# Kernel tuning notes

Hardware: AMD Instinct MI355X
Metric: run time of the kernel (lower is better)

Reference implementation:

```python
import jax, jax.numpy as jnp
import numpy as np

H = 64        # hidden_size
G = 64        # global_hidden_size
VOCAB = 128   # VOCAB_SIZE
NUM_OPS = 20
DEPTH = 12    # complete binary tree: 2**DEPTH - 1 nodes
B = 128       # batch of trees
TEMP = 3.0    # self.temperature


def setup_inputs() -> dict:
    key = jax.random.key(0)
    ks = jax.random.split(key, 16)
    s = 0.05
    N = 2 ** DEPTH - 1
    inp = {
        "x_idx": jax.random.randint(ks[0], (B, N), 0, VOCAB, dtype=jnp.int32),
        "validity_mask": jnp.ones((NUM_OPS,), jnp.float32),
        # binary tree-LSTM (blstm): x one-hot -> gates [i, f_a, f_b, o, u]
        "Wx": jax.random.normal(ks[1], (VOCAB, 5 * H), jnp.float32) * s,
        "Ua": jax.random.normal(ks[2], (H, 5 * H), jnp.float32) * s,
        "Ub": jax.random.normal(ks[3], (H, 5 * H), jnp.float32) * s,
        "b_tree": jnp.zeros((5 * H,), jnp.float32),
        # global nn.LSTM (1 layer), gate order i,f,g,o
        "W_ih": jax.random.normal(ks[4], (H, 4 * G), jnp.float32) * s,
        "W_hh": jax.random.normal(ks[5], (G, 4 * G), jnp.float32) * s,
        "b_lstm": jnp.zeros((4 * G,), jnp.float32),
        # FFN on root hidden
        "W1": jax.random.normal(ks[6], (H, H), jnp.float32) * s,
        "b1": jnp.zeros((H,), jnp.float32),
        "W2": jax.random.normal(ks[7], (H, H), jnp.float32) * s,
        "b2": jnp.zeros((H,), jnp.float32),
        # actor head on [hidden ; global_hidden]
        "actor_W": jax.random.normal(ks[8], (H + G, NUM_OPS), jnp.float32) * s,
        "actor_b": jnp.zeros((NUM_OPS,), jnp.float32),
    }
    return inp


def _tree_lstm_sweep(x_idx, Wx, Ua, Ub, b_tree):
    """Bottom-up binary tree-LSTM over a complete binary tree.
    Node i's children sit at flat positions 2i+1, 2i+2 (level layout)."""
    h_prev = c_prev = None
    for d in range(DEPTH - 1, -1, -1):
        n = 2 ** d
        off = n - 1
        # memory-bound gather of gate pre-activations: [B, n, 5H]
        z = Wx[x_idx[:, off:off + n]] + b_tree
        if h_prev is not None:
            h_a, h_b = h_prev[:, 0::2], h_prev[:, 1::2]
            c_a, c_b = c_prev[:, 0::2], c_prev[:, 1::2]
            z = z + jnp.einsum("bnh,hg->bng", h_a, Ua) + jnp.einsum("bnh,hg->bng", h_b, Ub)
        i, fa, fb, o, u = jnp.split(z, 5, axis=-1)
        c = jax.nn.sigmoid(i) * jnp.tanh(u)
        if h_prev is not None:
            c = c + jax.nn.sigmoid(fa) * c_a + jax.nn.sigmoid(fb) * c_b
        h = jax.nn.sigmoid(o) * jnp.tanh(c)
        h_prev, c_prev = h, c
    return h_prev[:, 0]  # root hidden [B, H]


def reference(x_idx, validity_mask, Wx, Ua, Ub, b_tree, W_ih, W_hh, b_lstm,
              W1, b1, W2, b2, actor_W, actor_b):
    h_root = _tree_lstm_sweep(x_idx, Wx, Ua, Ub, b_tree)
    # internal op 1: apply_ffn then apply_global_lstm
    f = jnp.maximum(h_root @ W1 + b1, 0.0) @ W2 + b2          # FFN [B, H]
    h0 = jnp.zeros((f.shape[0], G), f.dtype)
    g = f @ W_ih + h0 @ W_hh + b_lstm                          # one LSTM step
    i, fg, gg, o = jnp.split(g, 4, axis=-1)                    # torch order i,f,g,o
    c_g = jax.nn.sigmoid(i) * jnp.tanh(gg)                     # c0 = 0
    h_g = jax.nn.sigmoid(o) * jnp.tanh(c_g)                    # [B, G]
    # external actor with validity-masked weights (as in policy())
    feats = jnp.concatenate([f, h_g], axis=-1)                 # [B, H+G]
    logits = jnp.log(validity_mask) + feats @ (actor_W * validity_mask) + actor_b * validity_mask
    return jax.nn.softmax(logits / TEMP, axis=-1)              # [B, NUM_OPS]
```

## Files before the change

kernel.cpp:

```cpp
#include <hip/hip_runtime.h>


typedef unsigned short u16;
typedef unsigned int   u32;
typedef __attribute__((ext_vector_type(8))) short  short8;
typedef __attribute__((ext_vector_type(4))) float  floatx4;

#define L2E  1.44269504f
#define L2E2 2.885390082f

__device__ __forceinline__ float frcp(float x) { return __fdividef(1.0f, x); }
__device__ __forceinline__ float fsig(float x) { return frcp(1.0f + __expf(-x)); }
__device__ __forceinline__ float ftanh(float x) {
    return 1.0f - 2.0f * frcp(__expf(2.0f * x) + 1.0f);
}
__device__ __forceinline__ u16 f2bfa(float x) {
    return (u16)((__float_as_uint(x) + 0x8000u) >> 16);
}
__device__ __forceinline__ float bflo(u32 cc) { return __uint_as_float(cc << 16); }
__device__ __forceinline__ float bfhi(u32 cc) { return __uint_as_float(cc & 0xFFFF0000u); }

__device__ __forceinline__ void lstm_gates(
    float zi, float zfa, float zfb, float zo, float zu,
    float ca, float cb, float& c, float& h)
{
    zi  = fmaxf(zi, -60.f);  zfa = fmaxf(zfa, -60.f);
    zfb = fmaxf(zfb, -60.f); zo  = fmaxf(zo, -60.f);
    zu  = fmaxf(zu, -60.f);
    float ei  = __builtin_amdgcn_exp2f(-zi);
    float efa = __builtin_amdgcn_exp2f(-zfa);
    float efb = __builtin_amdgcn_exp2f(-zfb);
    float eo  = __builtin_amdgcn_exp2f(-zo);
    float eu2 = __builtin_amdgcn_exp2f(-zu);
    float pfa = 1.f + efa, pfb = 1.f + efb;
    float cf = (ca * pfb + cb * pfa) * __builtin_amdgcn_rcpf(pfa * pfb);
    c = (1.f - eu2) * __builtin_amdgcn_rcpf((1.f + ei) * (1.f + eu2)) + cf;
    float ec2 = __builtin_amdgcn_exp2f(fminf(-c * L2E2, 80.f));
    h = (1.f - ec2) * __builtin_amdgcn_rcpf((1.f + eo) * (1.f + ec2));
}

#define HS 72

__global__ void precompute_kernel(
    const float* __restrict__ Wx, const float* __restrict__ b_tree,
    const float* __restrict__ Ua, const float* __restrict__ Ub,
    float4* __restrict__ WpA, float* __restrict__ WpU,
    float4* __restrict__ TaA, float2* __restrict__ TaUC,
    float4* __restrict__ TbA, float2* __restrict__ TbUC,
    u16* __restrict__ Uswz)
{
    int v = blockIdx.x;
    int t = threadIdx.x;
    __shared__ float sz[320], sta[320], stb[320], sh[64], sc[64];
    float z = Wx[v * 320 + t] + b_tree[t];
    sz[t] = z;
    {
        int f = v * 320 + t;
        int j = f & 7, lane = (f >> 3) & 63, tk = f >> 9;
        int nt = tk % 20, kc = tk / 20;
        int k = kc * 32 + (lane >> 4) * 8 + j;
        int nn = nt * 16 + (lane & 15);
        float uval = (k < 64) ? Ua[k * 320 + nn] : Ub[(k - 64) * 320 + nn];
        uval *= ((nn >> 6) == 4) ? L2E2 : L2E;
        Uswz[f] = (u16)((__float_as_uint(uval) + 0x7FFFu +
                         ((__float_as_uint(uval) >> 16) & 1u)) >> 16);
    }
    __syncthreads();
    if (t < 64) {
        float c = fsig(sz[t]) * ftanh(sz[256 + t]);
        float h = fsig(sz[192 + t]) * ftanh(c);
        sc[t] = c; sh[t] = h;
    }
    __syncthreads();
    float ta = 0.f, tb = 0.f;
    #pragma unroll 8
    for (int k = 0; k < 64; ++k) {
        ta += sh[k] * Ua[k * 320 + t];
        tb += sh[k] * Ub[k * 320 + t];
    }
    sta[t] = ta; stb[t] = tb;
    __syncthreads();
    if (t < 64) {
        int o = (v << 6) + t;
        WpA[o]  = make_float4(sz[t] * L2E, sz[64 + t] * L2E,
                              sz[128 + t] * L2E, sz[192 + t] * L2E);
        WpU[o]  = sz[256 + t] * L2E2;
        TaA[o]  = make_float4(sta[t] * L2E, sta[64 + t] * L2E,
                              sta[128 + t] * L2E, sta[192 + t] * L2E);
        TaUC[o] = make_float2(sta[256 + t] * L2E2, sc[t]);
        TbA[o]  = make_float4(stb[t] * L2E, stb[64 + t] * L2E,
                              stb[128 + t] * L2E, stb[192 + t] * L2E);
        TbUC[o] = make_float2(stb[256 + t] * L2E2, sc[t]);
    }
}

template<int NT, int MODE, int GSRC>
__device__ __forceinline__ void sweep_level(
    const u16* hsrc, const u32* csrc,
    u16* hdst, u16* cdst, u16* hg, u16* cg, float* hroot,
    const short8 Bfrag[4][5],
    const float4* __restrict__ WpA, const float* __restrict__ WpU,
    const int* ids, int lbase, int node0g, int nvalid,
    int lane15, int quad, int wg)
{
    floatx4 acc[NT][5];
    #pragma unroll
    for (int mt = 0; mt < NT; ++mt)
        #pragma unroll
        for (int g = 0; g < 5; ++g) acc[mt][g] = (floatx4){0.f, 0.f, 0.f, 0.f};

    #pragma unroll
    for (int mt = 0; mt < NT; ++mt) {
        #pragma unroll
        for (int kc = 0; kc < 4; ++kc) {
            int child = 2 * (lbase + mt * 16 + lane15) + (kc >> 1);
            const u16* ap = GSRC ? (hsrc + child * 64 + (kc & 1) * 32 + quad * 8)
                                 : (hsrc + child * HS + (kc & 1) * 32 + quad * 8);
            short8 a = *(const short8*)ap;
            #pragma unroll
            for (int g = 0; g < 5; ++g)
                acc[mt][g] = __builtin_amdgcn_mfma_f32_16x16x32_bf16(
                    a, Bfrag[kc][g], acc[mt][g], 0, 0, 0);
        }
    }
    int hh = wg * 16 + lane15;
    #pragma unroll
    for (int mt = 0; mt < NT; ++mt) {
        #pragma unroll
        for (int r = 0; r < 4; ++r) {
            int lrow = lbase + mt * 16 + quad * 4 + r;
            int id = ids[lrow];
            float4 wgv = WpA[(id << 6) + hh];
            float  wu  = WpU[(id << 6) + hh];
            u32 cc = csrc[lrow * 64 + hh];
            float c, h;
            lstm_gates(acc[mt][0][r] + wgv.x, acc[mt][1][r] + wgv.y,
                       acc[mt][2][r] + wgv.z, acc[mt][3][r] + wgv.w,
                       acc[mt][4][r] + wu, bflo(cc), bfhi(cc), c, h);
            if (MODE == 0) {
                hdst[lrow * HS + hh] = f2bfa(h);
                cdst[(lrow >> 1) * 128 + hh * 2 + (lrow & 1)] = f2bfa(c);
            }
            if (MODE == 1) {
                if (lrow < nvalid) {
                    int node = node0g + lrow;
                    hg[node * 64 + hh] = f2bfa(h);
                    cg[(node >> 1) * 128 + hh * 2 + (node & 1)] = f2bfa(c);
                }
            }
            if (MODE == 2) {
                if (lrow == 0) hroot[hh] = h;
            }
        }
    }
}

__device__ __forceinline__ void load_bfrags(short8 Bfrag[4][5],
                                            const u16* __restrict__ Uswz,
                                            int wg, int lane)
{
    #pragma unroll
    for (int kc = 0; kc < 4; ++kc)
        #pragma unroll
        for (int g = 0; g < 5; ++g) {
            int nt = g * 4 + wg;
            Bfrag[kc][g] = *(const short8*)(Uswz + ((kc * 20 + nt) * 64 + lane) * 8);
        }
}

__global__ __launch_bounds__(512, 2) void sweepA_kernel(
    const int* __restrict__ x_idx,
    const float4* __restrict__ WpA, const float* __restrict__ WpU,
    const float4* __restrict__ TaA, const float2* __restrict__ TaUC,
    const float4* __restrict__ TbA, const float2* __restrict__ TbUC,
    const u16* __restrict__ Uswz,
    u16* __restrict__ h3, u16* __restrict__ c3)
{
    __shared__ u16 hA[128 * HS];
    __shared__ u16 cA[64 * 128];
    __shared__ u16 hB[64 * HS];
    __shared__ u16 cB[32 * 128];
    __shared__ int sIds[544];
    int t = threadIdx.x, lane = t & 63, wv = t >> 6;
    int wg = wv & 3, wm = wv >> 2;
    int lane15 = lane & 15, quad = lane >> 4;
    int b = blockIdx.x >> 3, st = blockIdx.x & 7;
    const int* xb = x_idx + b * 4095;

    for (int i = t; i < 544; i += 512) {
        int g;
        if      (i < 128) g = 1023 + st * 128 + i;
        else if (i < 384) g = 2047 + st * 256 + (i - 128);
        else if (i < 448) g = 511 + st * 64 + (i - 384);
        else if (i < 480) g = 255 + st * 32 + (i - 448);
        else if (i < 496) g = 127 + st * 16 + (i - 480);
        else if (i < 504) g = 63 + st * 8 + (i - 496);
        else if (i < 508) g = 31 + st * 4 + (i - 504);
        else if (i < 510) g = 15 + st * 2 + (i - 508);
        else if (i == 510) g = 7 + st;
        else g = -1;
        sIds[i] = (g >= 0) ? xb[g] : 0;
    }
    __syncthreads();

    #pragma unroll 4
    for (int rr = 0; rr < 16; ++rr) {
        int rl = wv * 16 + rr;
        int id = sIds[rl], ida = sIds[128 + 2 * rl], idb = sIds[129 + 2 * rl];
        float4 wgv = WpA[(id << 6) + lane];  float  wu = WpU[(id << 6) + lane];
        float4 ga = TaA[(ida << 6) + lane];  float2 ua = TaUC[(ida << 6) + lane];
        float4 gb = TbA[(idb << 6) + lane];  float2 ub = TbUC[(idb << 6) + lane];
        float c, h;
        lstm_gates(wgv.x + ga.x + gb.x, wgv.y + ga.y + gb.y, wgv.z + ga.z + gb.z,
                   wgv.w + ga.w + gb.w, wu + ua.x + ub.x, ua.y, ub.y, c, h);
        hA[rl * HS + lane] = f2bfa(h);
        cA[(rl >> 1) * 128 + lane * 2 + (rl & 1)] = f2bfa(c);
    }
    short8 Bfrag[4][5];
    load_bfrags(Bfrag, Uswz, wg, lane);
    __syncthreads();
    sweep_level<2, 0, 0>(hA, (const u32*)cA, hB, cB, nullptr, nullptr, nullptr,
                         Bfrag, WpA, WpU, &sIds[384], wm * 32, 0, 64, lane15, quad, wg);
    __syncthreads();
    sweep_level<1, 0, 0>(hB, (const u32*)cB, hA, cA, nullptr, nullptr, nullptr,
                         Bfrag, WpA, WpU, &sIds[448], wm * 16, 0, 32, lane15, quad, wg);
    __syncthreads();
    if (wm == 0)
        sweep_level<1, 0, 0>(hA, (const u32*)cA, hB, cB, nullptr, nullptr, nullptr,
                             Bfrag, WpA, WpU, &sIds[480], 0, 0, 16, lane15, quad, wg);
    __syncthreads();
    if (wm == 0)
        sweep_level<1, 0, 0>(hB, (const u32*)cB, hA, cA, nullptr, nullptr, nullptr,
                             Bfrag, WpA, WpU, &sIds[496], 0, 0, 8, lane15, quad, wg);
    __syncthreads();
    if (wm == 0)
        sweep_level<1, 0, 0>(hA, (const u32*)cA, hB, cB, nullptr, nullptr, nullptr,
                             Bfrag, WpA, WpU, &sIds[504], 0, 0, 4, lane15, quad, wg);
    __syncthreads();
    if (wm == 0)
        sweep_level<1, 0, 0>(hB, (const u32*)cB, hA, cA, nullptr, nullptr, nullptr,
                             Bfrag, WpA, WpU, &sIds[508], 0, 0, 2, lane15, quad, wg);
    __syncthreads();
    if (wm == 0)
        sweep_level<1, 1, 0>(hA, (const u32*)cA, nullptr, nullptr,
                             h3 + (size_t)b * 512, c3 + (size_t)b * 512, nullptr,
                             Bfrag, WpA, WpU, &sIds[510], 0, st, 1, lane15, quad, wg);
}

__global__ __launch_bounds__(256, 2) void sweepB_kernel(
    const int* __restrict__ x_idx,
    const float4* __restrict__ WpA, const float* __restrict__ WpU,
    const u16* __restrict__ Uswz,
    const u16* __restrict__ h3, const u16* __restrict__ c3,
    const float* __restrict__ W1, const float* __restrict__ b1,
    const float* __restrict__ W2, const float* __restrict__ b2,
    const float* __restrict__ W_ih, const float* __restrict__ b_lstm,
    const float* __restrict__ actor_W, const float* __restrict__ actor_b,
    const float* __restrict__ vm, float* __restrict__ out)
{
    __shared__ u16 hA[32 * HS];
    __shared__ u16 cA[16 * 128];
    __shared__ u16 hB[32 * HS];
    __shared__ u16 cB[16 * 128];
    __shared__ int sIds[32];
    __shared__ float hroot[64];
    int t = threadIdx.x, lane = t & 63, wv = t >> 6;
    int lane15 = lane & 15, quad = lane >> 4;
    int b = blockIdx.x;
    const int* xb = x_idx + b * 4095;
    const u16* h3b = h3 + (size_t)b * 512;
    const u16* c3b = c3 + (size_t)b * 512;

    if (t < 32) sIds[t] = (t < 31) ? xb[t] : 0;
    short8 Bfrag[4][5];
    load_bfrags(Bfrag, Uswz, wv, lane);
    __syncthreads();
    sweep_level<1, 0, 1>(h3b, (const u32*)c3b, hB, cB, nullptr, nullptr, nullptr,
                         Bfrag, WpA, WpU, &sIds[3], 0, 0, 4, lane15, quad, wv);
    __syncthreads();
    sweep_level<1, 0, 0>(hB, (const u32*)cB, hA, cA, nullptr, nullptr, nullptr,
                         Bfrag, WpA, WpU, &sIds[1], 0, 0, 2, lane15, quad, wv);
    __syncthreads();
    sweep_level<1, 2, 0>(hA, (const u32*)cA, nullptr, nullptr, nullptr, nullptr,
                         hroot, Bfrag, WpA, WpU, &sIds[0], 0, 0, 1, lane15, quad, wv);
    __syncthreads();

    if (wv == 0) {
        float a = b1[lane];
        #pragma unroll 8
        for (int k = 0; k < 64; ++k) a += hroot[k] * W1[k * 64 + lane];
        float r1 = fmaxf(a, 0.f);
        float f = b2[lane];
        #pragma unroll 8
        for (int k = 0; k < 64; ++k) f += __shfl(r1, k) * W2[k * 64 + lane];
        float gi = b_lstm[lane], gg = b_lstm[128 + lane], go = b_lstm[192 + lane];
        #pragma unroll 8
        for (int k = 0; k < 64; ++k) {
            float fk = __shfl(f, k);
            gi += fk * W_ih[k * 256 + lane];
            gg += fk * W_ih[k * 256 + 128 + lane];
            go += fk * W_ih[k * 256 + 192 + lane];
        }
        float cg = fsig(gi) * ftanh(gg);
        float hg = fsig(go) * ftanh(cg);
        int tt = (lane < 20) ? lane : 19;
        float dot = 0.f;
        #pragma unroll 8
        for (int k = 0; k < 64; ++k) {
            float fk = __shfl(f, k), hk = __shfl(hg, k);
            dot += fk * actor_W[k * 20 + tt] + hk * actor_W[(64 + k) * 20 + tt];
        }
        float m = vm[tt];
        float lg = logf(m) + dot * m + actor_b[tt] * m;
        float mx = -1e30f;
        #pragma unroll
        for (int j = 0; j < 20; ++j) mx = fmaxf(mx, __shfl(lg, j));
        float s = 0.f;
        #pragma unroll
        for (int j = 0; j < 20; ++j) s += __expf((__shfl(lg, j) - mx) * (1.0f / 3.0f));
        if (lane < 20) out[b * 20 + lane] = __expf((lg - mx) * (1.0f / 3.0f)) / s;
    }
}

extern "C" void kernel_launch(void* const* d_in, const int* in_sizes, int n_in,
                              void* d_out, int out_size, void* d_ws, size_t ws_size,
                              hipStream_t stream)
{
    const int*   x_idx   = (const int*)d_in[0];
    const float* vm      = (const float*)d_in[1];
    const float* Wx      = (const float*)d_in[2];
    const float* Ua      = (const float*)d_in[3];
    const float* Ub      = (const float*)d_in[4];
    const float* b_tree  = (const float*)d_in[5];
    const float* W_ih    = (const float*)d_in[6];
    const float* b_lstm  = (const float*)d_in[8];
    const float* W1      = (const float*)d_in[9];
    const float* b1      = (const float*)d_in[10];
    const float* W2      = (const float*)d_in[11];
    const float* b2      = (const float*)d_in[12];
    const float* actor_W = (const float*)d_in[13];
    const float* actor_b = (const float*)d_in[14];
    float* out = (float*)d_out;

    char* ws = (char*)d_ws;
    float4* WpA  = (float4*)ws;  ws += 128 * 64 * 16;
    float4* TaA  = (float4*)ws;  ws += 128 * 64 * 16;
    float4* TbA  = (float4*)ws;  ws += 128 * 64 * 16;
    float2* TaUC = (float2*)ws;  ws += 128 * 64 * 8;
    float2* TbUC = (float2*)ws;  ws += 128 * 64 * 8;
    float*  WpU  = (float*)ws;   ws += 128 * 64 * 4;
    u16*    h3   = (u16*)ws;     ws += 128 * 512 * 2;
    u16*    c3   = (u16*)ws;     ws += 128 * 512 * 2;
    u16*    Uswz = (u16*)ws;     ws += 128 * 320 * 2;

    precompute_kernel<<<128, 320, 0, stream>>>(Wx, b_tree, Ua, Ub,
                                               WpA, WpU, TaA, TaUC, TbA, TbUC, Uswz);
    sweepA_kernel<<<1024, 512, 0, stream>>>(x_idx, WpA, WpU, TaA, TaUC,
                                            TbA, TbUC, Uswz, h3, c3);
    sweepB_kernel<<<128, 256, 0, stream>>>(x_idx, WpA, WpU, Uswz, h3, c3,
                                           W1, b1, W2, b2, W_ih, b_lstm,
                                           actor_W, actor_b, vm, out);
}
```

Measured before the change: 158.7 us.

## Replace MFMA top-level sweep with single-wave fp32 scalar recurrence

The final three tree levels (4, 2 and 1 nodes per tree) are now computed by a single 64-lane wave per tree. Each lane owns one hidden unit and does fp32 dot products against a transposed fp32 U matrix, which the precompute kernel now writes out, instead of running bf16 MFMA fragments across four waves. The goal is to cut the setup cost of fragment loading, the block-wide syncs and the wasted MFMA tile work on these tiny levels. The trade-off is serial per-node loops with about 128x5 FMAs per lane, reading U from global memory or cache, and only one wave per block.

Measured after the change: 254.3 us. +60.3%, slower.

```diff
diff --git a/kernel.cpp b/kernel.cpp
--- a/kernel.cpp
+++ b/kernel.cpp
@@ -19,6 +19,7 @@
 }
 __device__ __forceinline__ float bflo(u32 cc) { return __uint_as_float(cc << 16); }
 __device__ __forceinline__ float bfhi(u32 cc) { return __uint_as_float(cc & 0xFFFF0000u); }
+__device__ __forceinline__ float bf2f(u16 s) { return __uint_as_float(((u32)s) << 16); }
 
 __device__ __forceinline__ void lstm_gates(
     float zi, float zfa, float zfb, float zo, float zu,
@@ -47,7 +48,7 @@
     float4* __restrict__ WpA, float* __restrict__ WpU,
     float4* __restrict__ TaA, float2* __restrict__ TaUC,
     float4* __restrict__ TbA, float2* __restrict__ TbUC,
-    u16* __restrict__ Uswz)
+    u16* __restrict__ Uswz, float* __restrict__ Ut)
 {
     int v = blockIdx.x;
     int t = threadIdx.x;
@@ -64,6 +65,12 @@
         uval *= ((nn >> 6) == 4) ? L2E2 : L2E;
         Uswz[f] = (u16)((__float_as_uint(uval) + 0x7FFFu +
                          ((__float_as_uint(uval) >> 16) & 1u)) >> 16);
+    }
+    {
+        int idx = v * 320 + t;
+        int c = idx >> 7, k = idx & 127;
+        float uval = (k < 64) ? Ua[k * 320 + c] : Ub[(k - 64) * 320 + c];
+        Ut[idx] = uval * (((c >> 6) == 4) ? L2E2 : L2E);
     }
     __syncthreads();
     if (t < 64) {
@@ -247,10 +254,10 @@
                              Bfrag, WpA, WpU, &sIds[510], 0, st, 1, lane15, quad, wg);
 }
 
-__global__ __launch_bounds__(256, 2) void sweepB_kernel(
+__global__ __launch_bounds__(64) void sweepB_kernel(
     const int* __restrict__ x_idx,
     const float4* __restrict__ WpA, const float* __restrict__ WpU,
-    const u16* __restrict__ Uswz,
+    const float* __restrict__ Ut,
     const u16* __restrict__ h3, const u16* __restrict__ c3,
     const float* __restrict__ W1, const float* __restrict__ b1,
     const float* __restrict__ W2, const float* __restrict__ b2,
@@ -258,37 +265,85 @@
     const float* __restrict__ actor_W, const float* __restrict__ actor_b,
     const float* __restrict__ vm, float* __restrict__ out)
 {
-    __shared__ u16 hA[32 * HS];
-    __shared__ u16 cA[16 * 128];
-    __shared__ u16 hB[32 * HS];
-    __shared__ u16 cB[16 * 128];
-    __shared__ int sIds[32];
-    __shared__ float hroot[64];
-    int t = threadIdx.x, lane = t & 63, wv = t >> 6;
-    int lane15 = lane & 15, quad = lane >> 4;
+    __shared__ float shA[8 * 64], scA[8 * 64];
+    __shared__ float shB[8 * 64], scB[8 * 64];
+    int lane = threadIdx.x;
     int b = blockIdx.x;
     const int* xb = x_idx + b * 4095;
     const u16* h3b = h3 + (size_t)b * 512;
     const u16* c3b = c3 + (size_t)b * 512;
 
-    if (t < 32) sIds[t] = (t < 31) ? xb[t] : 0;
-    short8 Bfrag[4][5];
-    load_bfrags(Bfrag, Uswz, wv, lane);
-    __syncthreads();
-    sweep_level<1, 0, 1>(h3b, (const u32*)c3b, hB, cB, nullptr, nullptr, nullptr,
-                         Bfrag, WpA, WpU, &sIds[3], 0, 0, 4, lane15, quad, wv);
-    __syncthreads();
-    sweep_level<1, 0, 0>(hB, (const u32*)cB, hA, cA, nullptr, nullptr, nullptr,
-                         Bfrag, WpA, WpU, &sIds[1], 0, 0, 2, lane15, quad, wv);
-    __syncthreads();
-    sweep_level<1, 2, 0>(hA, (const u32*)cA, nullptr, nullptr, nullptr, nullptr,
-                         hroot, Bfrag, WpA, WpU, &sIds[0], 0, 0, 1, lane15, quad, wv);
-    __syncthreads();
-
-    if (wv == 0) {
+    #pragma unroll
+    for (int n = 0; n < 8; ++n) {
+        shA[n * 64 + lane] = bf2f(h3b[n * 64 + lane]);
+        scA[n * 64 + lane] = bf2f(c3b[(n >> 1) * 128 + lane * 2 + (n & 1)]);
+    }
+    const float* u0 = Ut + (0 * 64 + lane) * 128;
+    const float* u1 = Ut + (1 * 64 + lane) * 128;
+    const float* u2 = Ut + (2 * 64 + lane) * 128;
+    const float* u3 = Ut + (3 * 64 + lane) * 128;
+    const float* u4 = Ut + (4 * 64 + lane) * 128;
+    __syncthreads();
+
+    float* srch = shA; float* srcc = scA;
+    float* dsth = shB; float* dstc = scB;
+    float hrootv = 0.f;
+    #pragma unroll
+    for (int lvl = 2; lvl >= 0; --lvl) {
+        int nrows = 1 << lvl;
+        int off = nrows - 1;
+        for (int r = 0; r < nrows; ++r) {
+            int id = xb[off + r];
+            float4 wgv = WpA[(id << 6) + lane];
+            float  wu  = WpU[(id << 6) + lane];
+            float zi = wgv.x, zfa = wgv.y, zfb = wgv.z, zo = wgv.w, zu = wu;
+            const float* hl = srch + (2 * r) * 64;
+            const float* hrr = srch + (2 * r + 1) * 64;
+            #pragma unroll
+            for (int k = 0; k < 64; k += 4) {
+                float4 a0 = *(const float4*)(u0 + k);
+                float4 a1 = *(const float4*)(u1 + k);
+                float4 a2 = *(const float4*)(u2 + k);
+                float4 a3 = *(const float4*)(u3 + k);
+                float4 a4 = *(const float4*)(u4 + k);
+                float h0 = hl[k], h1 = hl[k + 1], h2 = hl[k + 2], h3v = hl[k + 3];
+                zi  += a0.x * h0 + a0.y * h1 + a0.z * h2 + a0.w * h3v;
+                zfa += a1.x * h0 + a1.y * h1 + a1.z * h2 + a1.w * h3v;
+                zfb += a2.x * h0 + a2.y * h1 + a2.z * h2 + a2.w * h3v;
+                zo  += a3.x * h0 + a3.y * h1 + a3.z * h2 + a3.w * h3v;
+                zu  += a4.x * h0 + a4.y * h1 + a4.z * h2 + a4.w * h3v;
+            }
+            #pragma unroll
+            for (int k = 0; k < 64; k += 4) {
+                float4 a0 = *(const float4*)(u0 + 64 + k);
+                float4 a1 = *(const float4*)(u1 + 64 + k);
+                float4 a2 = *(const float4*)(u2 + 64 + k);
+                float4 a3 = *(const float4*)(u3 + 64 + k);
+                float4 a4 = *(const float4*)(u4 + 64 + k);
+                float h0 = hrr[k], h1 = hrr[k + 1], h2 = hrr[k + 2], h3v = hrr[k + 3];
+                zi  += a0.x * h0 + a0.y * h1 + a0.z * h2 + a0.w * h3v;
+                zfa += a1.x * h0 + a1.y * h1 + a1.z * h2 + a1.w * h3v;
+                zfb += a2.x * h0 + a2.y * h1 + a2.z * h2 + a2.w * h3v;
+                zo  += a3.x * h0 + a3.y * h1 + a3.z * h2 + a3.w * h3v;
+                zu  += a4.x * h0 + a4.y * h1 + a4.z * h2 + a4.w * h3v;
+            }
+            float c, h;
+            lstm_gates(zi, zfa, zfb, zo, zu,
+                       srcc[(2 * r) * 64 + lane], srcc[(2 * r + 1) * 64 + lane],
+                       c, h);
+            if (lvl == 0) hrootv = h;
+            else { dsth[r * 64 + lane] = h; dstc[r * 64 + lane] = c; }
+        }
+        __syncthreads();
+        float* tmp;
+        tmp = srch; srch = dsth; dsth = tmp;
+        tmp = srcc; srcc = dstc; dstc = tmp;
+    }
+
+    {
         float a = b1[lane];
         #pragma unroll 8
-        for (int k = 0; k < 64; ++k) a += hroot[k] * W1[k * 64 + lane];
+        for (int k = 0; k < 64; ++k) a += __shfl(hrootv, k) * W1[k * 64 + lane];
         float r1 = fmaxf(a, 0.f);
         float f = b2[lane];
         #pragma unroll 8
@@ -349,15 +404,17 @@
     float2* TaUC = (float2*)ws;  ws += 128 * 64 * 8;
     float2* TbUC = (float2*)ws;  ws += 128 * 64 * 8;
     float*  WpU  = (float*)ws;   ws += 128 * 64 * 4;
+    float*  Ut   = (float*)ws;   ws += 320 * 128 * 4;
     u16*    h3   = (u16*)ws;     ws += 128 * 512 * 2;
     u16*    c3   = (u16*)ws;     ws += 128 * 512 * 2;
     u16*    Uswz = (u16*)ws;     ws += 128 * 320 * 2;
 
     precompute_kernel<<<128, 320, 0, stream>>>(Wx, b_tree, Ua, Ub,
-                                               WpA, WpU, TaA, TaUC, TbA, TbUC, Uswz);
+                                               WpA, WpU, TaA, TaUC, TbA, TbUC,
+                                               Uswz, Ut);
     sweepA_kernel<<<1024, 512, 0, stream>>>(x_idx, WpA, WpU, TaA, TaUC,
                                             TbA, TbUC, Uswz, h3, c3);
-    sweepB_kernel<<<128, 256, 0, stream>>>(x_idx, WpA, WpU, Uswz, h3, c3,
-                                           W1, b1, W2, b2, W_ih, b_lstm,
-                                           actor_W, actor_b, vm, out);
-}
+    sweepB_kernel<<<128, 64, 0, stream>>>(x_idx, WpA, WpU, Ut, h3, c3,
+                                          W1, b1, W2, b2, W_ih, b_lstm,
+                                          actor_W, actor_b, vm, out);
+}
```

## Replace MFMA top-level sweep with single-wave fp32 dot-product kernel

Applied to the files above, without the earlier changes.

The final kernel, which handles the top three tree levels (4, 2 and 1 nodes per tree), no longer runs bf16 MFMA tiles across 4 waves. It now uses one 64-lane wave per tree doing plain fp32 FMA dot products. The precompute kernel writes an extra fp32 copy of the scaled Ua/Ub weights for this path. The goal is to stop paying for MFMA fragment loads, padding and multi-wave syncs on tiny row counts, and the root hidden state now reaches the FFN through a wave shuffle. In exchange, each lane streams 128x5 weights from global memory per level, serially, which may be latency-bound.

Measured after the change: 179.4 us. +13.1%, slower.

```diff
diff --git a/kernel.cpp b/kernel.cpp
--- a/kernel.cpp
+++ b/kernel.cpp
@@ -19,6 +19,7 @@
 }
 __device__ __forceinline__ float bflo(u32 cc) { return __uint_as_float(cc << 16); }
 __device__ __forceinline__ float bfhi(u32 cc) { return __uint_as_float(cc & 0xFFFF0000u); }
+__device__ __forceinline__ float bf2f(u16 s) { return __uint_as_float(((u32)s) << 16); }
 
 __device__ __forceinline__ void lstm_gates(
     float zi, float zfa, float zfb, float zo, float zu,
@@ -47,7 +48,7 @@
     float4* __restrict__ WpA, float* __restrict__ WpU,
     float4* __restrict__ TaA, float2* __restrict__ TaUC,
     float4* __restrict__ TbA, float2* __restrict__ TbUC,
-    u16* __restrict__ Uswz)
+    u16* __restrict__ Uswz, float* __restrict__ Us)
 {
     int v = blockIdx.x;
     int t = threadIdx.x;
@@ -64,6 +65,10 @@
         uval *= ((nn >> 6) == 4) ? L2E2 : L2E;
         Uswz[f] = (u16)((__float_as_uint(uval) + 0x7FFFu +
                          ((__float_as_uint(uval) >> 16) & 1u)) >> 16);
+    }
+    {
+        float uval = (v < 64) ? Ua[v * 320 + t] : Ub[(v - 64) * 320 + t];
+        Us[v * 320 + t] = uval * ((t >= 256) ? L2E2 : L2E);
     }
     __syncthreads();
     if (t < 64) {
@@ -247,10 +252,47 @@
                              Bfrag, WpA, WpU, &sIds[510], 0, st, 1, lane15, quad, wg);
 }
 
-__global__ __launch_bounds__(256, 2) void sweepB_kernel(
+template<int NR>
+__device__ __forceinline__ void dot_level(
+    const float* __restrict__ Us, const float4* __restrict__ WpA,
+    const float* __restrict__ WpU, const int* __restrict__ xb,
+    const float* srch, const float* srcc,
+    float* dsth, float* dstc, float* hrootv, int lane)
+{
+    int off = NR - 1;
+    float z[NR][5];
+    #pragma unroll
+    for (int r = 0; r < NR; ++r) {
+        int id = xb[off + r];
+        float4 wgv = WpA[(id << 6) + lane];
+        z[r][0] = wgv.x; z[r][1] = wgv.y; z[r][2] = wgv.z; z[r][3] = wgv.w;
+        z[r][4] = WpU[(id << 6) + lane];
+    }
+    #pragma unroll 4
+    for (int k = 0; k < 128; ++k) {
+        const float* uk = Us + k * 320 + lane;
+        float u0 = uk[0], u1 = uk[64], u2 = uk[128], u3 = uk[192], u4 = uk[256];
+        #pragma unroll
+        for (int r = 0; r < NR; ++r) {
+            float hk = srch[(2 * r + (k >> 6)) * 64 + (k & 63)];
+            z[r][0] += u0 * hk; z[r][1] += u1 * hk; z[r][2] += u2 * hk;
+            z[r][3] += u3 * hk; z[r][4] += u4 * hk;
+        }
+    }
+    #pragma unroll
+    for (int r = 0; r < NR; ++r) {
+        float c, h;
+        lstm_gates(z[r][0], z[r][1], z[r][2], z[r][3], z[r][4],
+                   srcc[(2 * r) * 64 + lane], srcc[(2 * r + 1) * 64 + lane], c, h);
+        if (NR == 1) *hrootv = h;
+        else { dsth[r * 64 + lane] = h; dstc[r * 64 + lane] = c; }
+    }
+}
+
+__global__ __launch_bounds__(64) void sweepB_kernel(
     const int* __restrict__ x_idx,
     const float4* __restrict__ WpA, const float* __restrict__ WpU,
-    const u16* __restrict__ Uswz,
+    const float* __restrict__ Us,
     const u16* __restrict__ h3, const u16* __restrict__ c3,
     const float* __restrict__ W1, const float* __restrict__ b1,
     const float* __restrict__ W2, const float* __restrict__ b2,
@@ -258,37 +300,32 @@
     const float* __restrict__ actor_W, const float* __restrict__ actor_b,
     const float* __restrict__ vm, float* __restrict__ out)
 {
-    __shared__ u16 hA[32 * HS];
-    __shared__ u16 cA[16 * 128];
-    __shared__ u16 hB[32 * HS];
-    __shared__ u16 cB[16 * 128];
-    __shared__ int sIds[32];
-    __shared__ float hroot[64];
-    int t = threadIdx.x, lane = t & 63, wv = t >> 6;
-    int lane15 = lane & 15, quad = lane >> 4;
+    __shared__ float shA[8 * 64], scA[8 * 64];
+    __shared__ float shB[4 * 64], scB[4 * 64];
+    int lane = threadIdx.x;
     int b = blockIdx.x;
     const int* xb = x_idx + b * 4095;
     const u16* h3b = h3 + (size_t)b * 512;
     const u16* c3b = c3 + (size_t)b * 512;
 
-    if (t < 32) sIds[t] = (t < 31) ? xb[t] : 0;
-    short8 Bfrag[4][5];
-    load_bfrags(Bfrag, Uswz, wv, lane);
-    __syncthreads();
-    sweep_level<1, 0, 1>(h3b, (const u32*)c3b, hB, cB, nullptr, nullptr, nullptr,
-                         Bfrag, WpA, WpU, &sIds[3], 0, 0, 4, lane15, quad, wv);
-    __syncthreads();
-    sweep_level<1, 0, 0>(hB, (const u32*)cB, hA, cA, nullptr, nullptr, nullptr,
-                         Bfrag, WpA, WpU, &sIds[1], 0, 0, 2, lane15, quad, wv);
-    __syncthreads();
-    sweep_level<1, 2, 0>(hA, (const u32*)cA, nullptr, nullptr, nullptr, nullptr,
-                         hroot, Bfrag, WpA, WpU, &sIds[0], 0, 0, 1, lane15, quad, wv);
-    __syncthreads();
-
-    if (wv == 0) {
+    #pragma unroll
+    for (int n = 0; n < 8; ++n) {
+        shA[n * 64 + lane] = bf2f(h3b[n * 64 + lane]);
+        scA[n * 64 + lane] = bf2f(c3b[(n >> 1) * 128 + lane * 2 + (n & 1)]);
+    }
+    __syncthreads();
+
+    float hrootv = 0.f;
+    dot_level<4>(Us, WpA, WpU, xb, shA, scA, shB, scB, nullptr, lane);
+    __syncthreads();
+    dot_level<2>(Us, WpA, WpU, xb, shB, scB, shA, scA, nullptr, lane);
+    __syncthreads();
+    dot_level<1>(Us, WpA, WpU, xb, shA, scA, nullptr, nullptr, &hrootv, lane);
+
+    {
         float a = b1[lane];
         #pragma unroll 8
-        for (int k = 0; k < 64; ++k) a += hroot[k] * W1[k * 64 + lane];
+        for (int k = 0; k < 64; ++k) a += __shfl(hrootv, k) * W1[k * 64 + lane];
         float r1 = fmaxf(a, 0.f);
         float f = b2[lane];
         #pragma unroll 8
@@ -349,15 +386,17 @@
     float2* TaUC = (float2*)ws;  ws += 128 * 64 * 8;
     float2* TbUC = (float2*)ws;  ws += 128 * 64 * 8;
     float*  WpU  = (float*)ws;   ws += 128 * 64 * 4;
+    float*  Us   = (float*)ws;   ws += 128 * 320 * 4;
     u16*    h3   = (u16*)ws;     ws += 128 * 512 * 2;
     u16*    c3   = (u16*)ws;     ws += 128 * 512 * 2;
     u16*    Uswz = (u16*)ws;     ws += 128 * 320 * 2;
 
     precompute_kernel<<<128, 320, 0, stream>>>(Wx, b_tree, Ua, Ub,
-                                               WpA, WpU, TaA, TaUC, TbA, TbUC, Uswz);
+                                               WpA, WpU, TaA, TaUC, TbA, TbUC,
+                                               Uswz, Us);
     sweepA_kernel<<<1024, 512, 0, stream>>>(x_idx, WpA, WpU, TaA, TaUC,
                                             TbA, TbUC, Uswz, h3, c3);
-    sweepB_kernel<<<128, 256, 0, stream>>>(x_idx, WpA, WpU, Uswz, h3, c3,
-                                           W1, b1, W2, b2, W_ih, b_lstm,
-                                           actor_W, actor_b, vm, out);
-}
+    sweepB_kernel<<<128, 64, 0, stream>>>(x_idx, WpA, WpU, Us, h3, c3,
+                                          W1, b1, W2, b2, W_ih, b_lstm,
+                                          actor_W, actor_b, vm, out);
+}
```
